# Performance work log

Hardware: AMD Instinct MI355X
Metric: run time of the kernel (lower is better)

The kernel has to match this reference:

```python
import jax, jax.numpy as jnp
import numpy as np
from jax import lax

COND, PRED, DH, NOUT = 64, 32, 128, 1
M, LQ, N, LR = 8, 256, 64, 512


def setup_inputs() -> dict:
    key = jax.random.key(0)
    ks = jax.random.split(key, 8)
    g = lambda k, sh, s=0.05: jax.random.normal(k, sh, jnp.float32) * s
    return {
        "query": jax.random.normal(ks[0], (M, LQ), jnp.float32),
        "ref": jax.random.normal(ks[1], (N, LR), jnp.float32),
        "q_weight": g(ks[2], (DH, 1, COND)),
        "q_bias": jnp.zeros((DH,), jnp.float32),
        "k_weight": g(ks[3], (DH, 1, COND)),
        "k_bias": jnp.zeros((DH,), jnp.float32),
        "v_weight": g(ks[4], (DH, 1, PRED), 0.1),
        "v_bias": jnp.zeros((DH,), jnp.float32),
        "m_weight": jnp.full((NOUT, 1, COND), 1.0 / COND, jnp.float32),
        "m_bias": jnp.zeros((NOUT,), jnp.float32),
        "o_weight": g(ks[5], (NOUT * PRED, DH), 0.1),
        "o_bias": jnp.zeros((NOUT * PRED,), jnp.float32),
        "m_key": g(ks[6], (1, 1, DH), 1.0),
    }


DN = ('NCH', 'OIH', 'NCH')


def _minmax_conv(x, w, b, offset=None, scale=None):
    # x: [B,1,L], w: [H,1,k] -> y: [B,H,W]. Each length-k window is min-max
    # normalized before the conv contraction. Since offset/scale are constant
    # per window: conv((x-off)/sc) = (conv(x) - off*sum(w)) / sc.
    k = w.shape[-1]
    if offset is None:
        offset = lax.reduce_window(x, jnp.inf, lax.min, (1, 1, k), (1, 1, 1), 'VALID')
    if scale is None:
        mx = lax.reduce_window(x, -jnp.inf, lax.max, (1, 1, k), (1, 1, 1), 'VALID')
        scale = mx - offset
        scale = jnp.where(scale == 0.0, 1.0, scale)
    raw = lax.conv_general_dilated(x, w, (1,), 'VALID', dimension_numbers=DN)
    wsum = w.sum(axis=(1, 2))
    y = (raw - offset * wsum[None, :, None]) / scale + b[None, :, None]
    return y, offset, scale


def reference(query, ref, q_weight, q_bias, k_weight, k_bias, v_weight, v_bias,
              m_weight, m_bias, o_weight, o_bias, m_key):
    cond, pred = q_weight.shape[-1], v_weight.shape[-1]
    # ---- query encoding ----
    q_in = jnp.cumsum(query, axis=1)[:, None, :]
    q, q_off, q_scale = _minmax_conv(q_in, q_weight, q_bias)
    q = q.transpose(0, 2, 1)                   # [M,Q,H]
    Qn = q.shape[1]
    q_scale_t = q_scale.transpose(0, 2, 1)     # [M,Q,1]
    qp = jnp.pad(query, ((0, 0), (cond - 1, 0)))[:, None, :]
    mc = lax.conv_general_dilated(qp, m_weight, (1,), 'VALID', dimension_numbers=DN)
    mc = mc + m_bias[None, :, None]
    mc = mc[..., cond - pred:]                 # [M,NOUT,Q+pred-1]
    widx = jnp.arange(pred)[:, None] + jnp.arange(Qn)[None, :]
    mwin = mc[..., widx]                       # [M,NOUT,pred,Q]
    m = mwin.reshape(mwin.shape[0], -1, Qn).transpose(0, 2, 1)  # [M,Q,NOUT*pred]
    m = m / q_scale_t
    # ---- key / value encoding ----
    k_in = jnp.cumsum(ref, axis=1)[:, None, :-pred]
    k, k_off, k_scale = _minmax_conv(k_in, k_weight, k_bias)
    k = k.transpose(0, 2, 1)                   # [N,K,H]
    v_in = ref[:, None, cond:]
    v, _, _ = _minmax_conv(v_in, v_weight, v_bias,
                           offset=jnp.zeros_like(k_off), scale=k_scale)
    v = v.transpose(0, 2, 1)                   # [N,K,H]
    # ---- scores ----
    full_score = jnp.einsum('mqh,nkh->mqkn', q, k)           # [M,Q,K,N]
    m_score = jnp.sum(q * m_key, axis=-1, keepdims=True)     # [M,Q,1]
    # ---- semi-hard attention: top-1 window per reference series ----
    ref_score = full_score.max(axis=2)         # [M,Q,N]
    max_idx = full_score.argmax(axis=2)        # [M,Q,N]
    n_ids = jnp.arange(v.shape[0])[None, None, :]
    sel_v = v[n_ids, max_idx]                  # [M,Q,N,H]
    sel_v = sel_v @ o_weight.T + o_bias        # [M,Q,N,D]
    scores = jax.nn.softmax(jnp.concatenate([ref_score, m_score], axis=-1), axis=-1)
    rs, ms = scores[..., :-1], scores[..., -1:]
    p = jnp.einsum('mqn,mqnd->mqd', rs, sel_v) + ms * m      # [M,Q,D]
    return p * q_scale_t
```

## Files before the change

kernel.cpp:

```cpp
#include <hip/hip_runtime.h>
#include <cmath>

#define M_B   8
#define LQ    256
#define N_B   64
#define LR    512
#define COND  64
#define PRED  32
#define DH    128
#define QN    193
#define KN    417
#define QPAD  256
#define KPAD  448

typedef _Float16 half8 __attribute__((ext_vector_type(8)));
typedef float f32x16 __attribute__((ext_vector_type(16)));

__device__ __forceinline__ f32x16 mfma_f16(half8 a, half8 b, f32x16 c) {
    return __builtin_amdgcn_mfma_f32_32x32x16_f16(a, b, c, 0, 0, 0);
}
__device__ __forceinline__ f32x16 zero16() {
    f32x16 z;
    #pragma unroll
    for (int i = 0; i < 16; i++) z[i] = 0.f;
    return z;
}

#define GLOAD_LDS16(g, l) __builtin_amdgcn_global_load_lds( \
    (const __attribute__((address_space(1))) void*)(g), \
    (__attribute__((address_space(3))) void*)(l), 16, 0, 0)

#define PIN_V(x) asm volatile("" : "+v"(x))

__launch_bounds__(256, 2)
__global__ void kA_feat(const float* __restrict__ query, const float* __restrict__ ref,
                        const float* __restrict__ qw, const float* __restrict__ qb,
                        const float* __restrict__ kw, const float* __restrict__ kb,
                        const float* __restrict__ vw, const float* __restrict__ vb,
                        float* __restrict__ q_scale, float* __restrict__ qfeat,
                        _Float16* __restrict__ qg,
                        _Float16* __restrict__ kg, float* __restrict__ vfeat) {
    __shared__ float x[512];
    __shared__ float buf[128 * 65];
    const int t = threadIdx.x;
    const int kl = t & 63;
    const int hq = __builtin_amdgcn_readfirstlane(t >> 6);

    if (blockIdx.x < 448) {
        const int n = blockIdx.x / 7, chunk = blockIdx.x % 7;
        x[t] = ref[n * 512 + t];
        x[t + 256] = ref[n * 512 + t + 256];
        __syncthreads();

        const int kp = chunk * 64 + kl;
        const bool vkp = kp < KN;
        float csw[64];
        float run = 0.f, mn = 0.f, mx = 0.f;
        csw[0] = 0.f;
        #pragma unroll
        for (int j = 1; j < 64; j++) {
            run += x[kp + j];
            csw[j] = run;
            mn = fminf(mn, run);
            mx = fmaxf(mx, run);
        }
        float scv = mx - mn; if (scv == 0.f) scv = 1.f;
        const float inv = 1.f / scv;
        #pragma unroll
        for (int j = 0; j < 64; j++) { csw[j] -= mn; PIN_V(csw[j]); }

        for (int hh = 0; hh < 32; hh++) {
            const int h = hq * 32 + hh;
            const float* wrow = kw + h * 64;
            float a0 = 0.f, a1 = 0.f, a2 = 0.f, a3 = 0.f;
            #pragma unroll
            for (int j = 0; j < 64; j += 4) {
                a0 = fmaf(wrow[j],     csw[j],     a0);
                a1 = fmaf(wrow[j + 1], csw[j + 1], a1);
                a2 = fmaf(wrow[j + 2], csw[j + 2], a2);
                a3 = fmaf(wrow[j + 3], csw[j + 3], a3);
            }
            float kraw = (a0 + a1) + (a2 + a3);
            float kval = vkp ? kraw * inv + kb[h] : 0.f;
            buf[h * 65 + (kl ^ (h >> 3))] = kval;
        }
        __syncthreads();
        {
            const size_t nb = ((size_t)n * KPAD + chunk * 64) * 256;
            #pragma unroll
            for (int r = 0; r < 8; r++) {
                int task = r * 256 + t;
                int kp_l = task >> 5, g = task & 31;
                int cb = g & 15, lo = g >> 4;
                half8 hv;
                #pragma unroll
                for (int jj = 0; jj < 8; jj++) {
                    float v = buf[(cb * 8 + jj) * 65 + (kp_l ^ cb)];
                    _Float16 hi = (_Float16)v;
                    hv[jj] = lo ? (_Float16)((v - (float)hi) * 1024.0f) : hi;
                }
                *(half8*)&kg[nb + (size_t)kp_l * 256 + ((size_t)(g ^ (kp_l & 31)) << 3)] = hv;
            }
        }
        __syncthreads();
        float refw[32];
        #pragma unroll
        for (int j = 0; j < 32; j++) {
            int ri = 64 + kp + j;
            refw[j] = (ri < 512) ? x[ri] : 0.f;
            PIN_V(refw[j]);
        }
        for (int hh = 0; hh < 32; hh++) {
            const int h = hq * 32 + hh;
            const float* vrow = vw + h * 32;
            float b0 = 0.f, b1 = 0.f;
            #pragma unroll
            for (int j = 0; j < 32; j += 2) {
                b0 = fmaf(vrow[j],     refw[j],     b0);
                b1 = fmaf(vrow[j + 1], refw[j + 1], b1);
            }
            float vval = vkp ? (b0 + b1) * inv + vb[h] : 0.f;
            buf[h * 65 + (kl ^ (h >> 3))] = vval;
        }
        __syncthreads();
        {
            const size_t vb0 = ((size_t)n * KPAD + chunk * 64) * 128;
            #pragma unroll
            for (int r = 0; r < 8; r++) {
                int idx = r * 256 + t;
                int kp_l = idx >> 5, c4 = idx & 31;
                float4 o;
                o.x = buf[(c4 * 4 + 0) * 65 + (kp_l ^ ((c4 * 4 + 0) >> 3))];
                o.y = buf[(c4 * 4 + 1) * 65 + (kp_l ^ ((c4 * 4 + 1) >> 3))];
                o.z = buf[(c4 * 4 + 2) * 65 + (kp_l ^ ((c4 * 4 + 2) >> 3))];
                o.w = buf[(c4 * 4 + 3) * 65 + (kp_l ^ ((c4 * 4 + 3) >> 3))];
                *(float4*)&vfeat[vb0 + (size_t)kp_l * 128 + c4 * 4] = o;
            }
        }
    } else {
        const int id = blockIdx.x - 448;
        const int m = id >> 2, qc = id & 3;
        x[t] = query[m * 256 + t];
        __syncthreads();

        const int qpos = qc * 64 + kl;
        const bool vq = qpos < QN;
        const int base = vq ? qpos : (QN - 1);
        float csw[64];
        float run = 0.f, mn = 0.f, mx = 0.f;
        csw[0] = 0.f;
        #pragma unroll
        for (int j = 1; j < 64; j++) {
            run += x[base + j];
            csw[j] = run;
            mn = fminf(mn, run);
            mx = fmaxf(mx, run);
        }
        float sc = mx - mn; if (sc == 0.f) sc = 1.f;
        const float inv = 1.f / sc;
        if (t < 64) q_scale[m * QPAD + qpos] = vq ? sc : 1.f;
        #pragma unroll
        for (int j = 0; j < 64; j++) { csw[j] -= mn; PIN_V(csw[j]); }

        for (int hh = 0; hh < 32; hh++) {
            const int h = hq * 32 + hh;
            const float* wrow = qw + h * 64;
            float a0 = 0.f, a1 = 0.f, a2 = 0.f, a3 = 0.f;
            #pragma unroll
            for (int j = 0; j < 64; j += 4) {
                a0 = fmaf(wrow[j],     csw[j],     a0);
                a1 = fmaf(wrow[j + 1], csw[j + 1], a1);
                a2 = fmaf(wrow[j + 2], csw[j + 2], a2);
                a3 = fmaf(wrow[j + 3], csw[j + 3], a3);
            }
            float raw = (a0 + a1) + (a2 + a3);
            float val = vq ? raw * inv + qb[h] : 0.f;
            buf[h * 65 + (kl ^ (h >> 3))] = val;
        }
        __syncthreads();
        const size_t qb0 = ((size_t)m * QPAD + qc * 64) * 128;
        #pragma unroll
        for (int r = 0; r < 8; r++) {
            int idx = r * 256 + t;
            int qp_l = idx >> 5, c4 = idx & 31;
            float4 o;
            o.x = buf[(c4 * 4 + 0) * 65 + (qp_l ^ ((c4 * 4 + 0) >> 3))];
            o.y = buf[(c4 * 4 + 1) * 65 + (qp_l ^ ((c4 * 4 + 1) >> 3))];
            o.z = buf[(c4 * 4 + 2) * 65 + (qp_l ^ ((c4 * 4 + 2) >> 3))];
            o.w = buf[(c4 * 4 + 3) * 65 + (qp_l ^ ((c4 * 4 + 3) >> 3))];
            *(float4*)&qfeat[qb0 + (size_t)qp_l * 128 + c4 * 4] = o;
        }
        #pragma unroll
        for (int r = 0; r < 8; r++) {
            int idx = r * 256 + t;
            int qp_l = idx >> 5, g = idx & 31;
            int c = g >> 2, kh = (g >> 1) & 1, lo = g & 1;
            half8 hv;
            #pragma unroll
            for (int jj = 0; jj < 8; jj++) {
                int h = c * 16 + kh * 8 + jj;
                float v = buf[h * 65 + (qp_l ^ (h >> 3))];
                _Float16 hi = (_Float16)v;
                hv[jj] = lo ? (_Float16)((v - (float)hi) * 1024.0f) : hi;
            }
            int qp2 = qc * 64 + qp_l;
            int grp = (m << 3) | (qp2 >> 5);
            size_t fb = (size_t)(grp * 16 + c * 2 + lo);
            *(half8*)&qg[fb * 512 + (size_t)(kh * 32 + (qp2 & 31)) * 8] = hv;
        }
    }
}

__launch_bounds__(256, 3)
__global__ void k3_score(const _Float16* __restrict__ qg, const _Float16* __restrict__ kg,
                         float* __restrict__ bscore, int* __restrict__ bidx) {
    __shared__ _Float16 Kbuf[2][32 * 256];
    const int blk = blockIdx.x;
    const int n = blk & 63, qt = blk >> 6;
    const int t = threadIdx.x, w = t >> 6, l = t & 63;
    const int lrow = l & 31, khalf = l >> 5;

    const int grp = qt * 4 + w;
    half8 qf[8][2];
    #pragma unroll
    for (int c = 0; c < 8; c++)
        #pragma unroll
        for (int h = 0; h < 2; h++)
            qf[c][h] = ((const half8*)qg)[(size_t)(grp * 16 + c * 2 + h) * 64 + l];

    const _Float16* ksrc = kg + (size_t)n * KPAD * 256;

    float best[16];
    unsigned bkt[2] = {0u, 0u};
    #pragma unroll
    for (int g = 0; g < 16; g++) best[g] = -INFINITY;

    #pragma unroll
    for (int rd = 0; rd < 4; rd++) {
        int e = (rd * 4 + w) * 512 + l * 8;
        GLOAD_LDS16(ksrc + e, &Kbuf[0][0] + e);
    }

    for (int kt = 0; kt < 14; kt++) {
        __syncthreads();
        if (kt < 13) {
            const _Float16* src = ksrc + (size_t)(kt + 1) * (32 * 256);
            _Float16* dst = &Kbuf[(kt + 1) & 1][0];
            #pragma unroll
            for (int rd = 0; rd < 4; rd++) {
                int e = (rd * 4 + w) * 512 + l * 8;
                GLOAD_LDS16(src + e, dst + e);
            }
        }
        const _Float16* krow = &Kbuf[kt & 1][0] + lrow * 256;
        f32x16 accH = zero16(), accL = zero16();
        half8 bh = *(const half8*)(krow + ((khalf ^ lrow) * 8));
        half8 bl = *(const half8*)(krow + (((16 + khalf) ^ lrow) * 8));
        #pragma unroll
        for (int c = 0; c < 8; c++) {
            half8 nbh, nbl;
            if (c < 7) {
                nbh = *(const half8*)(krow + ((((c + 1) * 2 + khalf) ^ lrow) * 8));
                nbl = *(const half8*)(krow + (((16 + (c + 1) * 2 + khalf) ^ lrow) * 8));
            }
            accH = mfma_f16(qf[c][0], bh, accH);
            accL = mfma_f16(qf[c][0], bl, accL);
            accL = mfma_f16(qf[c][1], bh, accL);
            bh = nbh; bl = nbl;
        }
        const int kp = kt * 32 + lrow;
        const bool valid = kp < KN;
        #pragma unroll
        for (int g = 0; g < 16; g++) {
            float sv = fmaf(accL[g], 0.0009765625f, accH[g]);
            if (valid && (sv > best[g])) {
                best[g] = sv;
                const unsigned sh = (unsigned)(g & 7) * 4u;
                bkt[g >> 3] = (bkt[g >> 3] & ~(0xFu << sh)) | ((unsigned)kt << sh);
            }
        }
    }

    #pragma unroll
    for (int g = 0; g < 16; g++) {
        float sv = best[g];
        int ktb = (int)((bkt[g >> 3] >> ((g & 7) * 4)) & 0xFu);
        int kp = ktb * 32 + lrow;
        for (int msk = 1; msk < 32; msk <<= 1) {
            float os = __shfl_xor(sv, msk, 64);
            int okp = __shfl_xor(kp, msk, 64);
            if (os > sv || (os == sv && okp < kp)) { sv = os; kp = okp; }
        }
        if (lrow == 0) {
            int row = (g & 3) + 8 * (g >> 2) + 4 * khalf;
            int mq = grp * 32 + row;
            if ((mq & 255) < QN) {
                bscore[(size_t)mq * 64 + n] = sv;
                bidx[(size_t)mq * 64 + n] = kp;
            }
        }
    }
}

__global__ void k4_out(const float* __restrict__ query,
                       const float* __restrict__ qfeat, const float* __restrict__ vfeat,
                       const float* __restrict__ bscore, const int* __restrict__ bidx,
                       const float* __restrict__ q_scale,
                       const float* __restrict__ mw, const float* __restrict__ mb,
                       const float* __restrict__ mkey,
                       const float* __restrict__ ow, const float* __restrict__ ob,
                       float* __restrict__ out) {
    __shared__ float rsS[4][64];
    __shared__ int   idxS[4][64];
    __shared__ float wS[4][128];
    const int t = threadIdx.x, wv = t >> 6, l = t & 63;
    const int j = blockIdx.x * 4 + wv;
    const int m = j / QN, qpos = j - m * QN;
    const int mq = m * QPAD + qpos;

    float s = bscore[(size_t)mq * 64 + l];
    int idx = bidx[(size_t)mq * 64 + l];
    float msv = qfeat[(size_t)mq * 128 + l] * mkey[l]
              + qfeat[(size_t)mq * 128 + 64 + l] * mkey[64 + l];
    #pragma unroll
    for (int msk = 1; msk < 64; msk <<= 1) msv += __shfl_xor(msv, msk, 64);
    float mx = s;
    #pragma unroll
    for (int msk = 1; msk < 64; msk <<= 1) mx = fmaxf(mx, __shfl_xor(mx, msk, 64));
    mx = fmaxf(mx, msv);
    float e = expf(s - mx);
    float sum = e;
    #pragma unroll
    for (int msk = 1; msk < 64; msk <<= 1) sum += __shfl_xor(sum, msk, 64);
    float ems = expf(msv - mx);
    float inv = 1.f / (sum + ems);
    float rs = e * inv, msw = ems * inv;

    rsS[wv][l] = rs; idxS[wv][l] = idx;
    __syncthreads();
    float ax = 0.f, ay = 0.f;
    #pragma unroll 8
    for (int nn = 0; nn < 64; nn++) {
        float r = rsS[wv][nn];
        int id = idxS[wv][nn];
        const float2 v = *(const float2*)&vfeat[((size_t)nn * KPAD + id) * 128 + 2 * l];
        ax = fmaf(r, v.x, ax);
        ay = fmaf(r, v.y, ay);
    }
    wS[wv][2 * l] = ax; wS[wv][2 * l + 1] = ay;
    __syncthreads();
    if (l < 32) {
        float p = 0.f;
        #pragma unroll
        for (int h4 = 0; h4 < 32; h4++) {
            const float4 wv4 = *(const float4*)&wS[wv][h4 * 4];
            const float4 o4 = *(const float4*)&ow[l * 128 + h4 * 4];
            p += wv4.x * o4.x + wv4.y * o4.y + wv4.z * o4.z + wv4.w * o4.w;
        }
        p += (1.f - msw) * ob[l];
        float mcv = mb[0];
        const int tpos = 32 + qpos + l;
        for (int jj = 0; jj < 64; jj++) {
            int qi = tpos + jj - 63;
            if (qi >= 0) mcv = fmaf(mw[jj], query[m * 256 + qi], mcv);
        }
        float outv = q_scale[mq] * p + msw * mcv;
        out[(size_t)j * 32 + l] = outv;
    }
}

extern "C" void kernel_launch(void* const* d_in, const int* in_sizes, int n_in,
                              void* d_out, int out_size, void* d_ws, size_t ws_size,
                              hipStream_t stream) {
    const float* query = (const float*)d_in[0];
    const float* ref   = (const float*)d_in[1];
    const float* qw    = (const float*)d_in[2];
    const float* qb    = (const float*)d_in[3];
    const float* kw    = (const float*)d_in[4];
    const float* kb    = (const float*)d_in[5];
    const float* vw    = (const float*)d_in[6];
    const float* vb    = (const float*)d_in[7];
    const float* mw    = (const float*)d_in[8];
    const float* mb    = (const float*)d_in[9];
    const float* ow    = (const float*)d_in[10];
    const float* ob    = (const float*)d_in[11];
    const float* mkey  = (const float*)d_in[12];
    float* out = (float*)d_out;

    float* ws = (float*)d_ws;
    float* q_scale = ws;
    float* qfeat   = ws + 2048;
    float* bscore  = ws + 264192;
    int*   bidx    = (int*)(ws + 395264);
    _Float16* qg   = (_Float16*)(ws + 526336);
    _Float16* kg   = (_Float16*)(ws + 788480);
    float* vfeat   = ws + 4458496;

    hipLaunchKernelGGL(kA_feat, dim3(480), dim3(256), 0, stream,
                       query, ref, qw, qb, kw, kb, vw, vb,
                       q_scale, qfeat, qg, kg, vfeat);
    hipLaunchKernelGGL(k3_score, dim3(1024), dim3(256), 0, stream,
                       qg, kg, bscore, bidx);
    hipLaunchKernelGGL(k4_out, dim3(386), dim3(256), 0, stream,
                       query, qfeat, vfeat, bscore, bidx, q_scale, mw, mb, mkey, ow, ob, out);
}
```

Measured before the change: 199.1 us.

## Pack query rows densely to skip padded score tiles and split output gather across waves

Query features are now packed contiguously across batches (1544 real rows instead of 8×256 padded rows), so the score kernel launches 832 blocks instead of 1024 and no longer computes tiles for padded query positions. The tail group is zeroed with a memset. The output kernel now handles one query row per block, with the 64-reference gather split across 4 waves using shuffles and an LDS reduction, which raises parallelism for the memory-bound gather. Best-index tracking in the score kernel uses per-row ints instead of packed nibbles. This adds an extra memset launch and more blocks in the output stage.

```diff
diff --git a/kernel.cpp b/kernel.cpp
--- a/kernel.cpp
+++ b/kernel.cpp
@@ -12,6 +12,8 @@
 #define KN    417
 #define QPAD  256
 #define KPAD  448
+#define QROWS 1544
+#define QGRPS 49
 
 typedef _Float16 half8 __attribute__((ext_vector_type(8)));
 typedef float f32x16 __attribute__((ext_vector_type(16)));
@@ -195,18 +197,21 @@
             int idx = r * 256 + t;
             int qp_l = idx >> 5, g = idx & 31;
             int c = g >> 2, kh = (g >> 1) & 1, lo = g & 1;
-            half8 hv;
-            #pragma unroll
-            for (int jj = 0; jj < 8; jj++) {
-                int h = c * 16 + kh * 8 + jj;
-                float v = buf[h * 65 + (qp_l ^ (h >> 3))];
-                _Float16 hi = (_Float16)v;
-                hv[jj] = lo ? (_Float16)((v - (float)hi) * 1024.0f) : hi;
-            }
             int qp2 = qc * 64 + qp_l;
-            int grp = (m << 3) | (qp2 >> 5);
-            size_t fb = (size_t)(grp * 16 + c * 2 + lo);
-            *(half8*)&qg[fb * 512 + (size_t)(kh * 32 + (qp2 & 31)) * 8] = hv;
+            if (qp2 < QN) {
+                half8 hv;
+                #pragma unroll
+                for (int jj = 0; jj < 8; jj++) {
+                    int h = c * 16 + kh * 8 + jj;
+                    float v = buf[h * 65 + (qp_l ^ (h >> 3))];
+                    _Float16 hi = (_Float16)v;
+                    hv[jj] = lo ? (_Float16)((v - (float)hi) * 1024.0f) : hi;
+                }
+                int prow = m * QN + qp2;
+                int grp = prow >> 5;
+                size_t fb = (size_t)(grp * 16 + c * 2 + lo);
+                *(half8*)&qg[fb * 512 + (size_t)(kh * 32 + (prow & 31)) * 8] = hv;
+            }
         }
     }
 }
@@ -231,9 +236,9 @@
     const _Float16* ksrc = kg + (size_t)n * KPAD * 256;
 
     float best[16];
-    unsigned bkt[2] = {0u, 0u};
-    #pragma unroll
-    for (int g = 0; g < 16; g++) best[g] = -INFINITY;
+    int bestkt[16];
+    #pragma unroll
+    for (int g = 0; g < 16; g++) { best[g] = -INFINITY; bestkt[g] = 0; }
 
     #pragma unroll
     for (int rd = 0; rd < 4; rd++) {
@@ -273,19 +278,14 @@
         #pragma unroll
         for (int g = 0; g < 16; g++) {
             float sv = fmaf(accL[g], 0.0009765625f, accH[g]);
-            if (valid && (sv > best[g])) {
-                best[g] = sv;
-                const unsigned sh = (unsigned)(g & 7) * 4u;
-                bkt[g >> 3] = (bkt[g >> 3] & ~(0xFu << sh)) | ((unsigned)kt << sh);
-            }
+            if (valid && (sv > best[g])) { best[g] = sv; bestkt[g] = kt; }
         }
     }
 
     #pragma unroll
     for (int g = 0; g < 16; g++) {
         float sv = best[g];
-        int ktb = (int)((bkt[g >> 3] >> ((g & 7) * 4)) & 0xFu);
-        int kp = ktb * 32 + lrow;
+        int kp = bestkt[g] * 32 + lrow;
         for (int msk = 1; msk < 32; msk <<= 1) {
             float os = __shfl_xor(sv, msk, 64);
             int okp = __shfl_xor(kp, msk, 64);
@@ -294,7 +294,7 @@
         if (lrow == 0) {
             int row = (g & 3) + 8 * (g >> 2) + 4 * khalf;
             int mq = grp * 32 + row;
-            if ((mq & 255) < QN) {
+            if (mq < QROWS) {
                 bscore[(size_t)mq * 64 + n] = sv;
                 bidx[(size_t)mq * 64 + n] = kp;
             }
@@ -310,16 +310,14 @@
                        const float* __restrict__ mkey,
                        const float* __restrict__ ow, const float* __restrict__ ob,
                        float* __restrict__ out) {
-    __shared__ float rsS[4][64];
-    __shared__ int   idxS[4][64];
-    __shared__ float wS[4][128];
+    __shared__ float pS[4][128];
     const int t = threadIdx.x, wv = t >> 6, l = t & 63;
-    const int j = blockIdx.x * 4 + wv;
+    const int j = blockIdx.x;
     const int m = j / QN, qpos = j - m * QN;
     const int mq = m * QPAD + qpos;
 
-    float s = bscore[(size_t)mq * 64 + l];
-    int idx = bidx[(size_t)mq * 64 + l];
+    float s = bscore[(size_t)j * 64 + l];
+    int idx = bidx[(size_t)j * 64 + l];
     float msv = qfeat[(size_t)mq * 128 + l] * mkey[l]
               + qfeat[(size_t)mq * 128 + 64 + l] * mkey[64 + l];
     #pragma unroll
@@ -336,24 +334,25 @@
     float inv = 1.f / (sum + ems);
     float rs = e * inv, msw = ems * inv;
 
-    rsS[wv][l] = rs; idxS[wv][l] = idx;
-    __syncthreads();
     float ax = 0.f, ay = 0.f;
-    #pragma unroll 8
-    for (int nn = 0; nn < 64; nn++) {
-        float r = rsS[wv][nn];
-        int id = idxS[wv][nn];
+    #pragma unroll
+    for (int k = 0; k < 16; k++) {
+        int nn = wv * 16 + k;
+        float r = __shfl(rs, nn, 64);
+        int  id = __shfl(idx, nn, 64);
         const float2 v = *(const float2*)&vfeat[((size_t)nn * KPAD + id) * 128 + 2 * l];
         ax = fmaf(r, v.x, ax);
         ay = fmaf(r, v.y, ay);
     }
-    wS[wv][2 * l] = ax; wS[wv][2 * l + 1] = ay;
+    pS[wv][2 * l] = ax; pS[wv][2 * l + 1] = ay;
     __syncthreads();
-    if (l < 32) {
+    if (t < 128) pS[0][t] = (pS[0][t] + pS[1][t]) + (pS[2][t] + pS[3][t]);
+    __syncthreads();
+    if (wv == 0 && l < 32) {
         float p = 0.f;
         #pragma unroll
         for (int h4 = 0; h4 < 32; h4++) {
-            const float4 wv4 = *(const float4*)&wS[wv][h4 * 4];
+            const float4 wv4 = *(const float4*)&pS[0][h4 * 4];
             const float4 o4 = *(const float4*)&ow[l * 128 + h4 * 4];
             p += wv4.x * o4.x + wv4.y * o4.y + wv4.z * o4.z + wv4.w * o4.w;
         }
@@ -396,11 +395,14 @@
     _Float16* kg   = (_Float16*)(ws + 788480);
     float* vfeat   = ws + 4458496;
 
+    hipMemsetAsync((void*)(qg + (size_t)768 * 512), 0,
+                   (size_t)64 * 512 * sizeof(_Float16), stream);
+
     hipLaunchKernelGGL(kA_feat, dim3(480), dim3(256), 0, stream,
                        query, ref, qw, qb, kw, kb, vw, vb,
                        q_scale, qfeat, qg, kg, vfeat);
-    hipLaunchKernelGGL(k3_score, dim3(1024), dim3(256), 0, stream,
+    hipLaunchKernelGGL(k3_score, dim3(832), dim3(256), 0, stream,
                        qg, kg, bscore, bidx);
-    hipLaunchKernelGGL(k4_out, dim3(386), dim3(256), 0, stream,
+    hipLaunchKernelGGL(k4_out, dim3(1544), dim3(256), 0, stream,
                        query, qfeat, vfeat, bscore, bidx, q_scale, mw, mb, mkey, ow, ob, out);
 }
```

Result: no change. 199.2 us (+0.0%).
